# Optimization experiments

Hardware: AMD Instinct MI355X
Metric: run time of the kernel (lower is better)

The kernel has to match this reference:

```python
import jax, jax.numpy as jnp
import numpy as np

N = 50000   # nodes
E = 800000  # edges (avg degree 16)
H = 128     # hidden


def setup_inputs() -> dict:
    key = jax.random.key(0)
    k1, k2, k3, k4, k5 = jax.random.split(key, 5)
    s = 1.0 / np.sqrt(H).astype(np.float32)
    x = jax.random.normal(k1, (N, H), dtype=jnp.float32)
    edge_index = jax.random.randint(k2, (2, E), 0, N, dtype=jnp.int64)
    a_i = jax.random.normal(k3, (H,), dtype=jnp.float32) * s
    a_j = jax.random.normal(k4, (H,), dtype=jnp.float32) * s
    W = jax.random.normal(k5, (H, H), dtype=jnp.float32) * s
    return {"x": x, "edge_index": edge_index, "a_i": a_i, "a_j": a_j, "W": W}


def reference(x, edge_index, a_i, a_j, W):
    n = x.shape[0]
    idx_j = edge_index[0]  # row of sparse adj (output node)
    idx_i = edge_index[1]  # col of sparse adj (source node, softmax segment)

    # per-node attention scores, gathered per edge
    si = x @ a_i  # [N]
    sj = x @ a_j  # [N]
    e = jax.nn.leaky_relu(si[idx_i] + sj[idx_j], negative_slope=0.01)  # [E]

    # segment softmax over idx_i (numerically stable)
    seg_max = jax.ops.segment_max(e, idx_i, num_segments=n)
    e_exp = jnp.exp(e - seg_max[idx_i])
    denom = jax.ops.segment_sum(e_exp, idx_i, num_segments=n)
    alpha = e_exp / denom[idx_i]  # [E]

    # messages and sparse aggregation: out[j] += alpha * m[i]
    m = x + x @ W  # [N, H]
    out = jax.ops.segment_sum(alpha[:, None] * m[idx_i], idx_j, num_segments=n)

    # exact (erf) GELU to match torch nn.GELU default; dropout is identity in eval
    return jax.nn.gelu(out, approximate=False)
```

## Files before the change

### kernel.cpp

```cpp
#include <hip/hip_runtime.h>
#include <hip/hip_fp16.h>
#include <math.h>

#define HDIM 128
#define DP   256
#define NB   64
#define CAP  1536
#define BINB 128

typedef __attribute__((ext_vector_type(8))) short short8;
typedef __attribute__((ext_vector_type(4))) float f32x4;

__device__ __forceinline__ float gelu_f(float v) {
    return 0.5f * v * (1.0f + erff(v * 0.70710678118654752440f));
}
__device__ __forceinline__ unsigned bf_rne(float f) {
    unsigned u = __float_as_uint(f);
    return (u + 0x7fffu + ((u >> 16) & 1u)) >> 16;
}
__device__ __forceinline__ float bf_lo(unsigned u) {
    return __uint_as_float(u << 16);
}
__device__ __forceinline__ float bf_hi(unsigned u) {
    return __uint_as_float(u & 0xffff0000u);
}

__global__ void __launch_bounds__(256) k_scores(
    const float* __restrict__ x, const float* __restrict__ a_i,
    const float* __restrict__ a_j, float* __restrict__ si,
    float* __restrict__ sj, unsigned* __restrict__ xbp,
    unsigned* __restrict__ gcnt, int N) {
    if (blockIdx.x == 0)
        for (int w = threadIdx.x; w < 1024; w += 256) gcnt[w] = 0u;
    const int wave = threadIdx.x >> 6;
    const int lane = threadIdx.x & 63;
    const int n = blockIdx.x * 4 + wave;
    if (n >= N) return;
    const float xa = x[(size_t)n * HDIM + lane];
    const float xb = x[(size_t)n * HDIM + 64 + lane];
    xbp[(size_t)n * 64 + lane] = bf_rne(xa) | (bf_rne(xb) << 16);
    float vi = xa * a_i[lane] + xb * a_i[64 + lane];
    float vj = xa * a_j[lane] + xb * a_j[64 + lane];
    #pragma unroll
    for (int d = 32; d; d >>= 1) {
        vi += __shfl_xor(vi, d, 64);
        vj += __shfl_xor(vj, d, 64);
    }
    if (lane == 0) {
        si[n] = vi;
        sj[n] = vj;
    }
}

__global__ void __launch_bounds__(1024) k_den(
    const int* __restrict__ idx_i, const int* __restrict__ idx_j,
    const float* __restrict__ si, const float* __restrict__ sj,
    unsigned short* __restrict__ exbuf, float* __restrict__ denp,
    int N, int E_) {
    __shared__ float den_l[12544];
    const int b = blockIdx.x;
    const int chunk = (E_ + DP - 1) / DP;
    const int e0 = b * chunk;
    const int e1 = min(e0 + chunk, E_);
    const int Q = (N + 3) >> 2;
    for (int pass = 0; pass < 4; ++pass) {
        const int lo = pass * Q;
        for (int w = threadIdx.x; w < Q; w += 1024) den_l[w] = 0.f;
        __syncthreads();
        for (int t = e0 + threadIdx.x; t < e1; t += 1024) {
            const int i = idx_i[t];
            float ex;
            if (pass == 0) {
                const int j = idx_j[t];
                float e = si[i] + sj[j];
                e = (e > 0.f) ? e : 0.01f * e;
                ex = __expf(e);
                exbuf[t] = __half_as_ushort(__float2half(ex));
            } else {
                ex = __half2float(__ushort_as_half(exbuf[t]));
            }
            const unsigned rel = (unsigned)(i - lo);
            if (rel < (unsigned)Q) atomicAdd(&den_l[rel], ex);
        }
        __syncthreads();
        for (int w = threadIdx.x; w < Q && lo + w < N; w += 1024)
            denp[(size_t)b * N + lo + w] = den_l[w];
        __syncthreads();
    }
}

__global__ void __launch_bounds__(256) k_denred(const float* __restrict__ denp,
                                                float* __restrict__ denom,
                                                int N) {
    const int v = blockIdx.x * 256 + threadIdx.x;
    if (v >= N) return;
    float s = 0.f;
    for (int b = 0; b < DP; ++b) s += denp[(size_t)b * N + v];
    denom[v] = s;
}

__global__ void __launch_bounds__(1024) k_bin(
    const int* __restrict__ idx_i, const int* __restrict__ idx_j,
    const unsigned short* __restrict__ exbuf, unsigned* __restrict__ gcnt,
    uint2* __restrict__ edges, int nbuk, int E_) {
    __shared__ unsigned cnt_l[1024];
    const int blk = blockIdx.x;
    const int chunk = (E_ + BINB - 1) / BINB;
    const int e0 = blk * chunk;
    const int e1 = min(e0 + chunk, E_);
    for (int w = threadIdx.x; w < nbuk; w += 1024) cnt_l[w] = 0u;
    __syncthreads();
    for (int t = e0 + threadIdx.x; t < e1; t += 1024)
        atomicAdd(&cnt_l[idx_j[t] >> 6], 1u);
    __syncthreads();
    for (int w = threadIdx.x; w < nbuk; w += 1024)
        cnt_l[w] = atomicAdd(&gcnt[w], cnt_l[w]);
    __syncthreads();
    for (int t = e0 + threadIdx.x; t < e1; t += 1024) {
        const int j = idx_j[t];
        const int b = j >> 6;
        const unsigned slot = min(atomicAdd(&cnt_l[b], 1u), (unsigned)(CAP - 1));
        const float ex = __half2float(__ushort_as_half(exbuf[t]));
        edges[(size_t)b * CAP + slot] = make_uint2(
            (unsigned)idx_i[t] | ((unsigned)(j & 63) << 24),
            __float_as_uint(ex));
    }
}

__global__ void __launch_bounds__(256) k_gemm(
    const unsigned* __restrict__ xbp, const float* __restrict__ Wm,
    const float* __restrict__ denom, unsigned* __restrict__ mbp, int N) {
    __shared__ unsigned wl[128][68];
    const int t = threadIdx.x;
    {
        const int n = t & 127;
        const int h = t >> 7;
        for (int w = h * 32; w < h * 32 + 32; ++w) {
            const float f0 = Wm[w * 128 + n];
            const float f1 = Wm[(w + 64) * 128 + n];
            wl[n][w] = bf_rne(f0) | (bf_rne(f1) << 16);
        }
    }
    __syncthreads();
    const int wave = t >> 6;
    const int lane = t & 63;
    const int q = lane >> 4;
    const int m16 = lane & 15;
    const int r0 = blockIdx.x * 64 + wave * 16;
    if (r0 >= N) return;
    const int rowA = min(r0 + m16, N - 1);
    union { uint4 u; short8 s; } a[4];
    #pragma unroll
    for (int kb = 0; kb < 4; ++kb)
        a[kb].u = *(const uint4*)(xbp + (size_t)rowA * 64 + kb * 16 + q * 4);
    f32x4 acc[8];
    #pragma unroll
    for (int c = 0; c < 8; ++c) acc[c] = (f32x4){0.f, 0.f, 0.f, 0.f};
    #pragma unroll
    for (int kb = 0; kb < 4; ++kb) {
        #pragma unroll
        for (int c = 0; c < 8; ++c) {
            const short8 bfr =
                *(const short8*)&wl[c * 16 + m16][kb * 16 + q * 4];
            acc[c] = __builtin_amdgcn_mfma_f32_16x16x32_bf16(
                a[kb].s, bfr, acc[c], 0, 0, 0);
        }
    }
    #pragma unroll
    for (int r = 0; r < 4; ++r) {
        const int row = r0 + q * 4 + r;
        if (row >= N) continue;
        const float rdv = 1.0f / denom[row];
        #pragma unroll
        for (int c = 0; c < 4; ++c) {
            const int w = m16 + 16 * c;
            const unsigned xv = xbp[(size_t)row * 64 + w];
            const float vlo = (bf_lo(xv) + acc[c][r]) * rdv;
            const float vhi = (bf_hi(xv) + acc[c + 4][r]) * rdv;
            mbp[(size_t)row * 64 + w] = bf_rne(vlo) | (bf_rne(vhi) << 16);
        }
    }
}

__global__ void __launch_bounds__(1024) k_agg(
    const unsigned* __restrict__ gcnt, const uint2* __restrict__ edges,
    const unsigned* __restrict__ mbp, float* __restrict__ out, int N) {
    __shared__ uint2 srec[CAP];
    __shared__ unsigned cnt_l[NB];
    __shared__ unsigned off_l[NB];
    const int b = blockIdx.x;
    const int cntb = min((int)gcnt[b], CAP);
    const uint2* eb = edges + (size_t)b * CAP;
    if (threadIdx.x < NB) cnt_l[threadIdx.x] = 0u;
    __syncthreads();
    uint2 rloc[2];
    int jloc[2], kloc[2], nmine = 0;
    for (int t = threadIdx.x; t < cntb; t += 1024) {
        const uint2 rec = eb[t];
        const int jrel = (int)(rec.x >> 24);
        const int rank = (int)atomicAdd(&cnt_l[jrel], 1u);
        rloc[nmine] = rec;
        jloc[nmine] = jrel;
        kloc[nmine] = rank;
        ++nmine;
    }
    __syncthreads();
    if (threadIdx.x < 64) {
        const unsigned v = cnt_l[threadIdx.x];
        unsigned s = v;
        #pragma unroll
        for (int d = 1; d < 64; d <<= 1) {
            const unsigned o = __shfl_up(s, d, 64);
            if ((int)threadIdx.x >= d) s += o;
        }
        off_l[threadIdx.x] = s - v;
    }
    __syncthreads();
    for (int k = 0; k < nmine; ++k)
        srec[off_l[jloc[k]] + kloc[k]] = rloc[k];
    __syncthreads();
    const int wave = threadIdx.x >> 6;
    const int lane = threadIdx.x & 63;
    for (int nr = wave; nr < NB; nr += 16) {
        const int n = (b << 6) + nr;
        if (n >= N) continue;
        const int p0 = (int)off_l[nr];
        const int p1 = p0 + (int)cnt_l[nr];
        float ax = 0.f, ay = 0.f;
        int p = p0;
        for (; p + 4 <= p1; p += 4) {
            const uint2 e0 = srec[p];
            const uint2 e1 = srec[p + 1];
            const uint2 e2 = srec[p + 2];
            const uint2 e3 = srec[p + 3];
            const unsigned u0 = mbp[(size_t)(e0.x & 0xffffffu) * 64 + lane];
            const unsigned u1 = mbp[(size_t)(e1.x & 0xffffffu) * 64 + lane];
            const unsigned u2 = mbp[(size_t)(e2.x & 0xffffffu) * 64 + lane];
            const unsigned u3 = mbp[(size_t)(e3.x & 0xffffffu) * 64 + lane];
            const float a0 = __uint_as_float(e0.y);
            const float a1 = __uint_as_float(e1.y);
            const float a2 = __uint_as_float(e2.y);
            const float a3 = __uint_as_float(e3.y);
            ax = fmaf(a0, bf_lo(u0), ax);
            ay = fmaf(a0, bf_hi(u0), ay);
            ax = fmaf(a1, bf_lo(u1), ax);
            ay = fmaf(a1, bf_hi(u1), ay);
            ax = fmaf(a2, bf_lo(u2), ax);
            ay = fmaf(a2, bf_hi(u2), ay);
            ax = fmaf(a3, bf_lo(u3), ax);
            ay = fmaf(a3, bf_hi(u3), ay);
        }
        for (; p < p1; ++p) {
            const uint2 e = srec[p];
            const unsigned u = mbp[(size_t)(e.x & 0xffffffu) * 64 + lane];
            const float a = __uint_as_float(e.y);
            ax = fmaf(a, bf_lo(u), ax);
            ay = fmaf(a, bf_hi(u), ay);
        }
        out[(size_t)n * HDIM + lane] = gelu_f(ax);
        out[(size_t)n * HDIM + 64 + lane] = gelu_f(ay);
    }
}

extern "C" void kernel_launch(void* const* d_in, const int* in_sizes, int n_in,
                              void* d_out, int out_size, void* d_ws,
                              size_t ws_size, hipStream_t stream) {
    const float* x   = (const float*)d_in[0];
    const int*   eix = (const int*)d_in[1];
    const float* a_i = (const float*)d_in[2];
    const float* a_j = (const float*)d_in[3];
    const float* Wm  = (const float*)d_in[4];
    float* out = (float*)d_out;

    const int N = in_sizes[0] / HDIM;
    const int E = in_sizes[1] / 2;
    const int nbuk = (N + NB - 1) / NB;

    unsigned* xbp  = (unsigned*)d_ws;
    unsigned* mbp  = xbp + (size_t)N * 64;
    float* denp    = (float*)(mbp + (size_t)N * 64);
    float* si      = denp + (size_t)DP * N;
    float* sj      = si + N;
    float* denom   = sj + N;
    unsigned* gcnt = (unsigned*)(denom + N);
    unsigned short* exbuf = (unsigned short*)(gcnt + 1024);
    uint2* edges   = (uint2*)(exbuf + E);

    const int* idx_j = eix;
    const int* idx_i = eix + E;

    k_scores<<<(N + 3) / 4, 256, 0, stream>>>(x, a_i, a_j, si, sj, xbp, gcnt,
                                              N);
    k_den<<<DP, 1024, 0, stream>>>(idx_i, idx_j, si, sj, exbuf, denp, N, E);
    k_denred<<<(N + 255) / 256, 256, 0, stream>>>(denp, denom, N);
    k_gemm<<<(N + 63) / 64, 256, 0, stream>>>(xbp, Wm, denom, mbp, N);
    k_bin<<<BINB, 1024, 0, stream>>>(idx_i, idx_j, exbuf, gcnt, edges, nbuk,
                                     E);
    k_agg<<<nbuk, 1024, 0, stream>>>(gcnt, edges, mbp, out, N);
}
```

Baseline: 197.0 us.

## Fuse softmax denominator into binning kernel with global atomics, shrink buckets

```diff
diff --git a/kernel.cpp b/kernel.cpp
--- a/kernel.cpp
+++ b/kernel.cpp
@@ -1,12 +1,10 @@
 #include <hip/hip_runtime.h>
-#include <hip/hip_fp16.h>
 #include <math.h>
 
 #define HDIM 128
-#define DP   256
-#define NB   64
-#define CAP  1536
-#define BINB 128
+#define NB   32
+#define CAP  768
+#define BINB 256
 
 typedef __attribute__((ext_vector_type(8))) short short8;
 typedef __attribute__((ext_vector_type(4))) float f32x4;
@@ -29,9 +27,9 @@
     const float* __restrict__ x, const float* __restrict__ a_i,
     const float* __restrict__ a_j, float* __restrict__ si,
     float* __restrict__ sj, unsigned* __restrict__ xbp,
-    unsigned* __restrict__ gcnt, int N) {
+    unsigned* __restrict__ gcnt, float* __restrict__ denom, int N) {
     if (blockIdx.x == 0)
-        for (int w = threadIdx.x; w < 1024; w += 256) gcnt[w] = 0u;
+        for (int w = threadIdx.x; w < 2048; w += 256) gcnt[w] = 0u;
     const int wave = threadIdx.x >> 6;
     const int lane = threadIdx.x & 63;
     const int n = blockIdx.x * 4 + wave;
@@ -49,81 +47,49 @@
     if (lane == 0) {
         si[n] = vi;
         sj[n] = vj;
-    }
-}
-
-__global__ void __launch_bounds__(1024) k_den(
+        denom[n] = 0.f;
+    }
+}
+
+__global__ void __launch_bounds__(1024) k_bin(
     const int* __restrict__ idx_i, const int* __restrict__ idx_j,
     const float* __restrict__ si, const float* __restrict__ sj,
-    unsigned short* __restrict__ exbuf, float* __restrict__ denp,
-    int N, int E_) {
-    __shared__ float den_l[12544];
-    const int b = blockIdx.x;
-    const int chunk = (E_ + DP - 1) / DP;
-    const int e0 = b * chunk;
-    const int e1 = min(e0 + chunk, E_);
-    const int Q = (N + 3) >> 2;
-    for (int pass = 0; pass < 4; ++pass) {
-        const int lo = pass * Q;
-        for (int w = threadIdx.x; w < Q; w += 1024) den_l[w] = 0.f;
-        __syncthreads();
-        for (int t = e0 + threadIdx.x; t < e1; t += 1024) {
-            const int i = idx_i[t];
-            float ex;
-            if (pass == 0) {
-                const int j = idx_j[t];
-                float e = si[i] + sj[j];
-                e = (e > 0.f) ? e : 0.01f * e;
-                ex = __expf(e);
-                exbuf[t] = __half_as_ushort(__float2half(ex));
-            } else {
-                ex = __half2float(__ushort_as_half(exbuf[t]));
-            }
-            const unsigned rel = (unsigned)(i - lo);
-            if (rel < (unsigned)Q) atomicAdd(&den_l[rel], ex);
-        }
-        __syncthreads();
-        for (int w = threadIdx.x; w < Q && lo + w < N; w += 1024)
-            denp[(size_t)b * N + lo + w] = den_l[w];
-        __syncthreads();
-    }
-}
-
-__global__ void __launch_bounds__(256) k_denred(const float* __restrict__ denp,
-                                                float* __restrict__ denom,
-                                                int N) {
-    const int v = blockIdx.x * 256 + threadIdx.x;
-    if (v >= N) return;
-    float s = 0.f;
-    for (int b = 0; b < DP; ++b) s += denp[(size_t)b * N + v];
-    denom[v] = s;
-}
-
-__global__ void __launch_bounds__(1024) k_bin(
-    const int* __restrict__ idx_i, const int* __restrict__ idx_j,
-    const unsigned short* __restrict__ exbuf, unsigned* __restrict__ gcnt,
+    float* __restrict__ denom, unsigned* __restrict__ gcnt,
     uint2* __restrict__ edges, int nbuk, int E_) {
-    __shared__ unsigned cnt_l[1024];
+    __shared__ unsigned cnt_l[2048];
     const int blk = blockIdx.x;
     const int chunk = (E_ + BINB - 1) / BINB;
     const int e0 = blk * chunk;
     const int e1 = min(e0 + chunk, E_);
     for (int w = threadIdx.x; w < nbuk; w += 1024) cnt_l[w] = 0u;
     __syncthreads();
-    for (int t = e0 + threadIdx.x; t < e1; t += 1024)
-        atomicAdd(&cnt_l[idx_j[t] >> 6], 1u);
-    __syncthreads();
-    for (int w = threadIdx.x; w < nbuk; w += 1024)
-        cnt_l[w] = atomicAdd(&gcnt[w], cnt_l[w]);
-    __syncthreads();
+    uint2 rec[4];
+    int   bloc[4];
+    int nmine = 0;
     for (int t = e0 + threadIdx.x; t < e1; t += 1024) {
+        const int i = idx_i[t];
         const int j = idx_j[t];
-        const int b = j >> 6;
+        float e = si[i] + sj[j];
+        e = (e > 0.f) ? e : 0.01f * e;
+        const float ex = __expf(e);
+        atomicAdd(&denom[i], ex);
+        const int b = j >> 5;
+        atomicAdd(&cnt_l[b], 1u);
+        rec[nmine] = make_uint2((unsigned)i | ((unsigned)(j & 31) << 24),
+                                __float_as_uint(ex));
+        bloc[nmine] = b;
+        ++nmine;
+    }
+    __syncthreads();
+    for (int w = threadIdx.x; w < nbuk; w += 1024) {
+        const unsigned c = cnt_l[w];
+        cnt_l[w] = c ? atomicAdd(&gcnt[w], c) : 0u;
+    }
+    __syncthreads();
+    for (int k = 0; k < nmine; ++k) {
+        const int b = bloc[k];
         const unsigned slot = min(atomicAdd(&cnt_l[b], 1u), (unsigned)(CAP - 1));
-        const float ex = __half2float(__ushort_as_half(exbuf[t]));
-        edges[(size_t)b * CAP + slot] = make_uint2(
-            (unsigned)idx_i[t] | ((unsigned)(j & 63) << 24),
-            __float_as_uint(ex));
+        edges[(size_t)b * CAP + slot] = rec[k];
     }
 }
 
@@ -182,7 +148,7 @@
     }
 }
 
-__global__ void __launch_bounds__(1024) k_agg(
+__global__ void __launch_bounds__(512) k_agg(
     const unsigned* __restrict__ gcnt, const uint2* __restrict__ edges,
     const unsigned* __restrict__ mbp, float* __restrict__ out, int N) {
     __shared__ uint2 srec[CAP];
@@ -195,7 +161,7 @@
     __syncthreads();
     uint2 rloc[2];
     int jloc[2], kloc[2], nmine = 0;
-    for (int t = threadIdx.x; t < cntb; t += 1024) {
+    for (int t = threadIdx.x; t < cntb; t += 512) {
         const uint2 rec = eb[t];
         const int jrel = (int)(rec.x >> 24);
         const int rank = (int)atomicAdd(&cnt_l[jrel], 1u);
@@ -205,11 +171,11 @@
         ++nmine;
     }
     __syncthreads();
-    if (threadIdx.x < 64) {
+    if (threadIdx.x < NB) {
         const unsigned v = cnt_l[threadIdx.x];
         unsigned s = v;
         #pragma unroll
-        for (int d = 1; d < 64; d <<= 1) {
+        for (int d = 1; d < NB; d <<= 1) {
             const unsigned o = __shfl_up(s, d, 64);
             if ((int)threadIdx.x >= d) s += o;
         }
@@ -221,13 +187,47 @@
     __syncthreads();
     const int wave = threadIdx.x >> 6;
     const int lane = threadIdx.x & 63;
-    for (int nr = wave; nr < NB; nr += 16) {
-        const int n = (b << 6) + nr;
+    for (int nr = wave; nr < NB; nr += 8) {
+        const int n = (b << 5) + nr;
         if (n >= N) continue;
         const int p0 = (int)off_l[nr];
         const int p1 = p0 + (int)cnt_l[nr];
         float ax = 0.f, ay = 0.f;
         int p = p0;
+        for (; p + 8 <= p1; p += 8) {
+            const uint2 e0 = srec[p];
+            const uint2 e1 = srec[p + 1];
+            const uint2 e2 = srec[p + 2];
+            const uint2 e3 = srec[p + 3];
+            const uint2 e4 = srec[p + 4];
+            const uint2 e5 = srec[p + 5];
+            const uint2 e6 = srec[p + 6];
+            const uint2 e7 = srec[p + 7];
+            const unsigned u0 = mbp[(size_t)(e0.x & 0xffffffu) * 64 + lane];
+            const unsigned u1 = mbp[(size_t)(e1.x & 0xffffffu) * 64 + lane];
+            const unsigned u2 = mbp[(size_t)(e2.x & 0xffffffu) * 64 + lane];
+            const unsigned u3 = mbp[(size_t)(e3.x & 0xffffffu) * 64 + lane];
+            const unsigned u4 = mbp[(size_t)(e4.x & 0xffffffu) * 64 + lane];
+            const unsigned u5 = mbp[(size_t)(e5.x & 0xffffffu) * 64 + lane];
+            const unsigned u6 = mbp[(size_t)(e6.x & 0xffffffu) * 64 + lane];
+            const unsigned u7 = mbp[(size_t)(e7.x & 0xffffffu) * 64 + lane];
+            ax = fmaf(__uint_as_float(e0.y), bf_lo(u0), ax);
+            ay = fmaf(__uint_as_float(e0.y), bf_hi(u0), ay);
+            ax = fmaf(__uint_as_float(e1.y), bf_lo(u1), ax);
+            ay = fmaf(__uint_as_float(e1.y), bf_hi(u1), ay);
+            ax = fmaf(__uint_as_float(e2.y), bf_lo(u2), ax);
+            ay = fmaf(__uint_as_float(e2.y), bf_hi(u2), ay);
+            ax = fmaf(__uint_as_float(e3.y), bf_lo(u3), ax);
+            ay = fmaf(__uint_as_float(e3.y), bf_hi(u3), ay);
+            ax = fmaf(__uint_as_float(e4.y), bf_lo(u4), ax);
+            ay = fmaf(__uint_as_float(e4.y), bf_hi(u4), ay);
+            ax = fmaf(__uint_as_float(e5.y), bf_lo(u5), ax);
+            ay = fmaf(__uint_as_float(e5.y), bf_hi(u5), ay);
+            ax = fmaf(__uint_as_float(e6.y), bf_lo(u6), ax);
+            ay = fmaf(__uint_as_float(e6.y), bf_hi(u6), ay);
+            ax = fmaf(__uint_as_float(e7.y), bf_lo(u7), ax);
+            ay = fmaf(__uint_as_float(e7.y), bf_hi(u7), ay);
+        }
         for (; p + 4 <= p1; p += 4) {
             const uint2 e0 = srec[p];
             const uint2 e1 = srec[p + 1];
@@ -237,18 +237,14 @@
             const unsigned u1 = mbp[(size_t)(e1.x & 0xffffffu) * 64 + lane];
             const unsigned u2 = mbp[(size_t)(e2.x & 0xffffffu) * 64 + lane];
             const unsigned u3 = mbp[(size_t)(e3.x & 0xffffffu) * 64 + lane];
-            const float a0 = __uint_as_float(e0.y);
-            const float a1 = __uint_as_float(e1.y);
-            const float a2 = __uint_as_float(e2.y);
-            const float a3 = __uint_as_float(e3.y);
-            ax = fmaf(a0, bf_lo(u0), ax);
-            ay = fmaf(a0, bf_hi(u0), ay);
-            ax = fmaf(a1, bf_lo(u1), ax);
-            ay = fmaf(a1, bf_hi(u1), ay);
-            ax = fmaf(a2, bf_lo(u2), ax);
-            ay = fmaf(a2, bf_hi(u2), ay);
-            ax = fmaf(a3, bf_lo(u3), ax);
-            ay = fmaf(a3, bf_hi(u3), ay);
+            ax = fmaf(__uint_as_float(e0.y), bf_lo(u0), ax);
+            ay = fmaf(__uint_as_float(e0.y), bf_hi(u0), ay);
+            ax = fmaf(__uint_as_float(e1.y), bf_lo(u1), ax);
+            ay = fmaf(__uint_as_float(e1.y), bf_hi(u1), ay);
+            ax = fmaf(__uint_as_float(e2.y), bf_lo(u2), ax);
+            ay = fmaf(__uint_as_float(e2.y), bf_hi(u2), ay);
+            ax = fmaf(__uint_as_float(e3.y), bf_lo(u3), ax);
+            ay = fmaf(__uint_as_float(e3.y), bf_hi(u3), ay);
         }
         for (; p < p1; ++p) {
             const uint2 e = srec[p];
@@ -278,23 +274,19 @@
 
     unsigned* xbp  = (unsigned*)d_ws;
     unsigned* mbp  = xbp + (size_t)N * 64;
-    float* denp    = (float*)(mbp + (size_t)N * 64);
-    float* si      = denp + (size_t)DP * N;
+    float* si      = (float*)(mbp + (size_t)N * 64);
     float* sj      = si + N;
     float* denom   = sj + N;
     unsigned* gcnt = (unsigned*)(denom + N);
-    unsigned short* exbuf = (unsigned short*)(gcnt + 1024);
-    uint2* edges   = (uint2*)(exbuf + E);
+    uint2* edges   = (uint2*)(gcnt + 2048);
 
     const int* idx_j = eix;
     const int* idx_i = eix + E;
 
     k_scores<<<(N + 3) / 4, 256, 0, stream>>>(x, a_i, a_j, si, sj, xbp, gcnt,
-                                              N);
-    k_den<<<DP, 1024, 0, stream>>>(idx_i, idx_j, si, sj, exbuf, denp, N, E);
-    k_denred<<<(N + 255) / 256, 256, 0, stream>>>(denp, denom, N);
+                                              denom, N);
+    k_bin<<<BINB, 1024, 0, stream>>>(idx_i, idx_j, si, sj, denom, gcnt, edges,
+                                     nbuk, E);
     k_gemm<<<(N + 63) / 64, 256, 0, stream>>>(xbp, Wm, denom, mbp, N);
-    k_bin<<<BINB, 1024, 0, stream>>>(idx_i, idx_j, exbuf, gcnt, edges, nbuk,
-                                     E);
-    k_agg<<<nbuk, 1024, 0, stream>>>(gcnt, edges, mbp, out, N);
-}
+    k_agg<<<nbuk, 512, 0, stream>>>(gcnt, edges, mbp, out, N);
+}
```

Result: faster. 192.5 us (-2.3%).
